# Performance work log

Measured on AMD Instinct MI355X. Metric: run time of the kernel, lower is better.

The kernel has to match this reference:

```python
import jax, jax.numpy as jnp
import numpy as np

DIM = 1024
HEADS = 16
DIM_HEAD = DIM // HEADS  # 64


def setup_inputs() -> dict:
    key = jax.random.key(0)
    k1, k2, k3 = jax.random.split(key, 3)
    x = jax.random.normal(k1, (4, 2048, DIM), dtype=jnp.float32)
    # Linear weights stored as [in, out] so y = x @ W (torch Linear uses x @ W.T; init is random either way)
    w_qkv = jax.random.normal(k2, (DIM, 3 * DIM), dtype=jnp.float32) * (DIM ** -0.5)
    w_out = jax.random.normal(k3, (DIM, DIM), dtype=jnp.float32) * (DIM ** -0.5)
    return {"x": x, "w_qkv": w_qkv, "w_out": w_out}


def reference(x, w_qkv, w_out):
    b, t, d = x.shape
    h, dh = HEADS, DIM_HEAD
    qkv = x @ w_qkv  # [b, t, 3*h*dh]
    q, k, v = jnp.split(qkv, 3, axis=-1)
    split_heads = lambda a: a.reshape(b, t, h, dh).transpose(0, 2, 1, 3)  # [b,h,t,dh]
    q, k, v = map(split_heads, (q, k, v))
    # NOTE: original scales by full model dim d, not per-head dim
    scale = d ** (-0.5)
    dots = jnp.einsum('bhie,bhje->bhij', q, k) * scale  # [b,h,t,t]
    attn = jax.nn.softmax(dots, axis=-1)
    out = jnp.einsum('bhij,bhje->bhie', attn, v)  # [b,h,t,dh]
    out = out.transpose(0, 2, 1, 3).reshape(b, t, h * dh)
    return out @ w_out
```

## Files before the change

kernel.cpp:

```cpp
#include <hip/hip_runtime.h>


typedef __bf16 bf16x8 __attribute__((ext_vector_type(8)));
typedef __bf16 bf16x4 __attribute__((ext_vector_type(4)));
typedef __bf16 bf16x2 __attribute__((ext_vector_type(2)));
typedef float f32x4 __attribute__((ext_vector_type(4)));
typedef float f32x2 __attribute__((ext_vector_type(2)));
typedef float f32x16 __attribute__((ext_vector_type(16)));
typedef unsigned short ushort8 __attribute__((ext_vector_type(8)));

#define MFMA16(a, b, c) __builtin_amdgcn_mfma_f32_16x16x32_bf16((a), (b), (c), 0, 0, 0)
#define MFMA32(a, b, c) __builtin_amdgcn_mfma_f32_32x32x16_bf16((a), (b), (c), 0, 0, 0)

__device__ __forceinline__ unsigned short f2bf(float f) {
  unsigned int u = __float_as_uint(f);
  u = (u + 0x7FFFu + ((u >> 16) & 1u)) >> 16;
  return (unsigned short)u;
}

__device__ __forceinline__ float fast_exp2(float x) {
#if __has_builtin(__builtin_amdgcn_exp2f)
  return __builtin_amdgcn_exp2f(x);
#else
  float r;
  asm("v_exp_f32 %0, %1" : "=v"(r) : "v"(x));
  return r;
#endif
}

__device__ __forceinline__ void gload_lds16(const unsigned short* g, unsigned short* l) {
  __builtin_amdgcn_global_load_lds(
      (const __attribute__((address_space(1))) unsigned int*)g,
      (__attribute__((address_space(3))) unsigned int*)l, 16, 0, 0);
}

__device__ __forceinline__ void half_swap(unsigned int a, unsigned int b,
                                          unsigned int& x, unsigned int& y,
                                          bool H) {
#if __has_builtin(__builtin_amdgcn_permlane32_swap)
  auto r = __builtin_amdgcn_permlane32_swap(a, b, false, false);
  x = (unsigned int)r[0];
  y = (unsigned int)r[1];
#else
  unsigned int oa = (unsigned int)__shfl_xor((int)a, 32);
  unsigned int ob = (unsigned int)__shfl_xor((int)b, 32);
  x = H ? ob : a;
  y = H ? b : oa;
#endif
}

__global__ __launch_bounds__(256) void prep_kernel(
    const float* __restrict__ x, unsigned short* __restrict__ xb,
    const float* __restrict__ wqkv, unsigned short* __restrict__ WqkvT,
    const float* __restrict__ wout, unsigned short* __restrict__ WoutT) {
  const int bid = blockIdx.x;
  const int tid = threadIdx.x;
  if (bid < 4096) {
    int i = (bid * 256 + tid) * 8;
    float4 a = *(const float4*)&x[i];
    float4 b = *(const float4*)&x[i + 4];
    ushort8 o = {f2bf(a.x), f2bf(a.y), f2bf(a.z), f2bf(a.w),
                 f2bf(b.x), f2bf(b.y), f2bf(b.z), f2bf(b.w)};
    *(ushort8*)&xb[i] = o;
    return;
  }
  __shared__ float t[32][33];
  const float* in;
  unsigned short* out;
  int C, scale_limit, c0, r0;
  if (bid < 4096 + 3072) {
    int tj = bid - 4096;
    in = wqkv; out = WqkvT; C = 3072; scale_limit = 1024;
    c0 = (tj % 96) * 32; r0 = (tj / 96) * 32;
  } else {
    int tj = bid - 7168;
    in = wout; out = WoutT; C = 1024; scale_limit = 0;
    c0 = (tj & 31) * 32; r0 = (tj >> 5) * 32;
  }
  const float kQScale = 0.045084220027780106f;
#pragma unroll
  for (int i = 0; i < 4; ++i) {
    int e = tid + i * 256;
    int r = e >> 5, c = e & 31;
    t[r][c] = in[(size_t)(r0 + r) * C + c0 + c];
  }
  __syncthreads();
#pragma unroll
  for (int i = 0; i < 4; ++i) {
    int e = tid + i * 256;
    int r = e >> 5, c = e & 31;
    float v = t[c][r];
    if (c0 + r < scale_limit) v *= kQScale;
    out[(size_t)(c0 + r) * 1024 + r0 + c] = f2bf(v);
  }
}

template <int MODE>
__global__ __launch_bounds__(256) void gemm_bt(
    const unsigned short* __restrict__ A, const unsigned short* __restrict__ Bt,
    void* __restrict__ Cv, unsigned short* __restrict__ VT,
    int M, int N, int K) {
  __shared__ unsigned short As[128 * 32];
  __shared__ unsigned short Bs[128 * 32];
  const int tid = threadIdx.x;
  const int wave = tid >> 6, lane = tid & 63;
  const int g = lane >> 4, ln = lane & 15;
  const int wm = wave >> 1, wn = wave & 1;
  const long bm = (long)blockIdx.y * 128;
  const long bn = (long)blockIdx.x * 128;

  f32x4 acc[4][4];
#pragma unroll
  for (int i = 0; i < 4; ++i)
#pragma unroll
    for (int j = 0; j < 4; ++j) acc[i][j] = (f32x4){0.f, 0.f, 0.f, 0.f};

  const int srow = wave * 32 + (lane >> 2);
  const int scol = (lane & 3) * 8;
  const unsigned short* gA0 = A + (bm + srow) * (long)K + scol;
  const unsigned short* gA1 = gA0 + 16 * (long)K;
  const unsigned short* gB0 = Bt + (bn + srow) * (long)K + scol;
  const unsigned short* gB1 = gB0 + 16 * (long)K;
  unsigned short* lA0 = &As[wave * 1024];
  unsigned short* lA1 = &As[wave * 1024 + 512];
  unsigned short* lB0 = &Bs[wave * 1024];
  unsigned short* lB1 = &Bs[wave * 1024 + 512];

  for (int k0 = 0; k0 < K; k0 += 32) {
    __syncthreads();
    gload_lds16(gA0 + k0, lA0);
    gload_lds16(gA1 + k0, lA1);
    gload_lds16(gB0 + k0, lB0);
    gload_lds16(gB1 + k0, lB1);
    __syncthreads();

    bf16x8 af[4], bfr[4];
#pragma unroll
    for (int i = 0; i < 4; ++i) {
      af[i]  = *(const bf16x8*)&As[(wm * 64 + i * 16 + ln) * 32 + g * 8];
      bfr[i] = *(const bf16x8*)&Bs[(wn * 64 + i * 16 + ln) * 32 + g * 8];
    }
    __builtin_amdgcn_s_setprio(1);
#pragma unroll
    for (int i = 0; i < 4; ++i)
#pragma unroll
      for (int j = 0; j < 4; ++j)
        acc[i][j] = MFMA16(af[i], bfr[j], acc[i][j]);
    __builtin_amdgcn_s_setprio(0);
  }

  const long crow = bm + wm * 64, ccol = bn + wn * 64;
  if (MODE == 2 && bn >= 2048) {
#pragma unroll
    for (int i = 0; i < 4; ++i)
#pragma unroll
      for (int j = 0; j < 4; ++j) {
        int nv = (int)(ccol + j * 16 + ln) - 2048;
        int h = nv >> 6, dh = nv & 63;
        long tg = crow + i * 16 + g * 4;
        int b = (int)(tg >> 11), tl = (int)(tg & 2047);
        size_t idx = (size_t)(b * 16 + h) * 131072 + (size_t)dh * 2048 + tl;
        bf16x4 o = {(__bf16)acc[i][j][0], (__bf16)acc[i][j][1],
                    (__bf16)acc[i][j][2], (__bf16)acc[i][j][3]};
        *(bf16x4*)&VT[idx] = o;
      }
  } else {
#pragma unroll
    for (int i = 0; i < 4; ++i)
#pragma unroll
      for (int j = 0; j < 4; ++j)
#pragma unroll
        for (int r = 0; r < 4; ++r) {
          long idx = (crow + i * 16 + g * 4 + r) * (long)N + ccol + j * 16 + ln;
          if (MODE == 1)
            ((float*)Cv)[idx] = acc[i][j][r];
          else
            ((unsigned short*)Cv)[idx] = f2bf(acc[i][j][r]);
        }
  }
}

__global__ __launch_bounds__(256, 2) void attn_kernel(
    const unsigned short* __restrict__ qkv, const unsigned short* __restrict__ VT,
    unsigned short* __restrict__ attn_out) {
  __shared__ unsigned short Ks[3][64][64];
  __shared__ unsigned short Vs[3][64][64];

  const int tid = threadIdx.x;
  const int wave = tid >> 6, lane = tid & 63;
  const int l31 = lane & 31, hb = lane >> 5;

  const int wg = (blockIdx.x & 7) * 64 + (blockIdx.x >> 3);
  const int bh = wg >> 3, qc = wg & 7;
  const int b = bh >> 4, head = bh & 15;
  const int q0 = qc * 256 + wave * 64;

  bf16x8 qfA[4], qfB[4];
  {
    size_t baseA = (size_t)(b * 2048 + q0 + l31) * 3072 + head * 64 + 8 * hb;
    size_t baseB = baseA + (size_t)32 * 3072;
    qfA[0] = *(const bf16x8*)&qkv[baseA];
    qfA[1] = *(const bf16x8*)&qkv[baseA + 16];
    qfA[2] = *(const bf16x8*)&qkv[baseA + 32];
    qfA[3] = *(const bf16x8*)&qkv[baseA + 48];
    qfB[0] = *(const bf16x8*)&qkv[baseB];
    qfB[1] = *(const bf16x8*)&qkv[baseB + 16];
    qfB[2] = *(const bf16x8*)&qkv[baseB + 32];
    qfB[3] = *(const bf16x8*)&qkv[baseB + 48];
  }

  f32x16 oaccA[2], oaccB[2];
#pragma unroll
  for (int i = 0; i < 16; ++i) {
    oaccA[0][i] = 0.f; oaccA[1][i] = 0.f;
    oaccB[0][i] = 0.f; oaccB[1][i] = 0.f;
  }
  f32x2 lsA = {0.f, 0.f}, lsB = {0.f, 0.f};

  const int srow = tid >> 3;
  const int sc = tid & 7;
  const int swz = (sc ^ (srow & 7)) * 8;
  const unsigned short* gK =
      qkv + (size_t)b * 2048 * 3072 + 1024 + head * 64 + (size_t)srow * 3072 + swz;
  const unsigned short* gV = VT + (size_t)bh * 131072 + (size_t)srow * 2048 + swz;
  const int wrow = wave * 8;

  auto STAGE = [&](int buf, int j) {
    gload_lds16(gK + (size_t)j * 3072,        &Ks[buf][wrow][0]);
    gload_lds16(gK + (size_t)(j + 32) * 3072, &Ks[buf][wrow + 32][0]);
    gload_lds16(gV + j,                       &Vs[buf][wrow][0]);
    gload_lds16(gV + 32 * 2048 + j,           &Vs[buf][wrow + 32][0]);
  };

  const int myx = l31 & 7;
  const bool H = (hb != 0);

  STAGE(0, 0);
  STAGE(1, 64);

  int idx = 0;
  for (int j0 = 0; j0 < 2048; j0 += 64) {
    if (j0 + 64 < 2048)
      asm volatile("s_waitcnt vmcnt(4)" ::: "memory");
    else
      asm volatile("s_waitcnt vmcnt(0)" ::: "memory");
    __builtin_amdgcn_s_barrier();
    __builtin_amdgcn_sched_barrier(0);
    if (j0 + 128 < 2048) {
      int nb = idx + 2; if (nb >= 3) nb -= 3;
      STAGE(nb, j0 + 128);
    }

#pragma unroll
    for (int kt = 0; kt < 2; ++kt) {
      f32x16 saA, saB;
#pragma unroll
      for (int i = 0; i < 16; ++i) { saA[i] = 0.f; saB[i] = 0.f; }
      __builtin_amdgcn_s_setprio(1);
#pragma unroll
      for (int t = 0; t < 4; ++t) {
        bf16x8 kf = *(const bf16x8*)&Ks[idx][kt * 32 + l31][((2 * t + hb) ^ myx) * 8];
        saA = MFMA32(kf, qfA[t], saA);
        saB = MFMA32(kf, qfB[t], saB);
      }
      __builtin_amdgcn_s_setprio(0);

      unsigned int pkwA[8], pkwB[8];
#pragma unroll
      for (int j = 0; j < 8; ++j) {
        float a0 = fast_exp2(saA[2 * j]);
        float a1 = fast_exp2(saA[2 * j + 1]);
        lsA += (f32x2){a0, a1};
        bf16x2 av = {(__bf16)a0, (__bf16)a1};
        pkwA[j] = __builtin_bit_cast(unsigned int, av);
        float b0 = fast_exp2(saB[2 * j]);
        float b1 = fast_exp2(saB[2 * j + 1]);
        lsB += (f32x2){b0, b1};
        bf16x2 bv = {(__bf16)b0, (__bf16)b1};
        pkwB[j] = __builtin_bit_cast(unsigned int, bv);
      }

      union { unsigned int u[4]; bf16x8 v; } pfA0, pfA1, pfB0, pfB1;
      half_swap(pkwA[0], pkwA[2], pfA0.u[0], pfA0.u[2], H);
      half_swap(pkwA[1], pkwA[3], pfA0.u[1], pfA0.u[3], H);
      half_swap(pkwA[4], pkwA[6], pfA1.u[0], pfA1.u[2], H);
      half_swap(pkwA[5], pkwA[7], pfA1.u[1], pfA1.u[3], H);
      half_swap(pkwB[0], pkwB[2], pfB0.u[0], pfB0.u[2], H);
      half_swap(pkwB[1], pkwB[3], pfB0.u[1], pfB0.u[3], H);
      half_swap(pkwB[4], pkwB[6], pfB1.u[0], pfB1.u[2], H);
      half_swap(pkwB[5], pkwB[7], pfB1.u[1], pfB1.u[3], H);

      __builtin_amdgcn_s_setprio(1);
#pragma unroll
      for (int mt = 0; mt < 2; ++mt) {
        bf16x8 vf0 = *(const bf16x8*)&Vs[idx][mt * 32 + l31][((4 * kt + hb) ^ myx) * 8];
        bf16x8 vf1 = *(const bf16x8*)&Vs[idx][mt * 32 + l31][((4 * kt + 2 + hb) ^ myx) * 8];
        oaccA[mt] = MFMA32(vf0, pfA0.v, oaccA[mt]);
        oaccA[mt] = MFMA32(vf1, pfA1.v, oaccA[mt]);
        oaccB[mt] = MFMA32(vf0, pfB0.v, oaccB[mt]);
        oaccB[mt] = MFMA32(vf1, pfB1.v, oaccB[mt]);
      }
      __builtin_amdgcn_s_setprio(0);
    }

    idx = (idx == 2) ? 0 : idx + 1;
  }

  {
    float l = lsA.x + lsA.y;
    l += __shfl_xor(l, 32);
    float inv = 1.0f / l;
    size_t row = (size_t)(b * 2048 + q0 + l31) * 1024 + head * 64;
#pragma unroll
    for (int mt = 0; mt < 2; ++mt)
#pragma unroll
      for (int rq = 0; rq < 4; ++rq) {
        bf16x4 o = {(__bf16)(oaccA[mt][4 * rq + 0] * inv),
                    (__bf16)(oaccA[mt][4 * rq + 1] * inv),
                    (__bf16)(oaccA[mt][4 * rq + 2] * inv),
                    (__bf16)(oaccA[mt][4 * rq + 3] * inv)};
        *(bf16x4*)&attn_out[row + mt * 32 + 8 * rq + 4 * hb] = o;
      }
  }
  {
    float l = lsB.x + lsB.y;
    l += __shfl_xor(l, 32);
    float inv = 1.0f / l;
    size_t row = (size_t)(b * 2048 + q0 + 32 + l31) * 1024 + head * 64;
#pragma unroll
    for (int mt = 0; mt < 2; ++mt)
#pragma unroll
      for (int rq = 0; rq < 4; ++rq) {
        bf16x4 o = {(__bf16)(oaccB[mt][4 * rq + 0] * inv),
                    (__bf16)(oaccB[mt][4 * rq + 1] * inv),
                    (__bf16)(oaccB[mt][4 * rq + 2] * inv),
                    (__bf16)(oaccB[mt][4 * rq + 3] * inv)};
        *(bf16x4*)&attn_out[row + mt * 32 + 8 * rq + 4 * hb] = o;
      }
  }
}

extern "C" void kernel_launch(void* const* d_in, const int* in_sizes, int n_in,
                              void* d_out, int out_size, void* d_ws, size_t ws_size,
                              hipStream_t stream) {
  (void)in_sizes; (void)n_in; (void)out_size; (void)ws_size;
  const float* x_f     = (const float*)d_in[0];
  const float* w_qkv_f = (const float*)d_in[1];
  const float* w_out_f = (const float*)d_in[2];
  float* out = (float*)d_out;

  char* ws = (char*)d_ws;
  unsigned short* qkv   = (unsigned short*)(ws);
  unsigned short* attn  = (unsigned short*)(ws + 50331648);
  unsigned short* VT    = (unsigned short*)(ws + 67108864);
  unsigned short* WqkvT = (unsigned short*)(ws + 83886080);
  unsigned short* WoutT = (unsigned short*)(ws + 90177536);
  unsigned short* xb    = (unsigned short*)(ws + 92274688);

  prep_kernel<<<8192, 256, 0, stream>>>(x_f, xb, w_qkv_f, WqkvT, w_out_f, WoutT);
  gemm_bt<2><<<dim3(24, 64), 256, 0, stream>>>(xb, WqkvT, qkv, VT, 8192, 3072, 1024);
  attn_kernel<<<512, 256, 0, stream>>>(qkv, VT, attn);
  gemm_bt<1><<<dim3(8, 64), 256, 0, stream>>>(attn, WoutT, out, nullptr, 8192, 1024, 1024);
}
```

Measured before the change: 183.3 us.

## Triple-buffer GEMM LDS tiles with async global-to-LDS prefetch

Replaces the single-buffered LDS tile loop in the bf16 GEMM with a three-stage ring buffer. Tiles are prefetched two k-steps ahead, with vmcnt waits and a single barrier per iteration instead of two, so global-to-LDS loads overlap the MFMA work. This triples the LDS footprint per block, which may lower occupancy, and depends on the vmcnt counting matching the four loads issued per stage.

```diff
diff --git a/kernel.cpp b/kernel.cpp
--- a/kernel.cpp
+++ b/kernel.cpp
@@ -100,8 +100,8 @@
     const unsigned short* __restrict__ A, const unsigned short* __restrict__ Bt,
     void* __restrict__ Cv, unsigned short* __restrict__ VT,
     int M, int N, int K) {
-  __shared__ unsigned short As[128 * 32];
-  __shared__ unsigned short Bs[128 * 32];
+  __shared__ unsigned short As[3 * 4096];
+  __shared__ unsigned short Bs[3 * 4096];
   const int tid = threadIdx.x;
   const int wave = tid >> 6, lane = tid & 63;
   const int g = lane >> 4, ln = lane & 15;
@@ -121,24 +121,37 @@
   const unsigned short* gA1 = gA0 + 16 * (long)K;
   const unsigned short* gB0 = Bt + (bn + srow) * (long)K + scol;
   const unsigned short* gB1 = gB0 + 16 * (long)K;
-  unsigned short* lA0 = &As[wave * 1024];
-  unsigned short* lA1 = &As[wave * 1024 + 512];
-  unsigned short* lB0 = &Bs[wave * 1024];
-  unsigned short* lB1 = &Bs[wave * 1024 + 512];
-
+
+  auto STAGE = [&](int buf, int k0) {
+    unsigned short* lA = &As[buf * 4096 + wave * 1024];
+    unsigned short* lB = &Bs[buf * 4096 + wave * 1024];
+    gload_lds16(gA0 + k0, lA);
+    gload_lds16(gA1 + k0, lA + 512);
+    gload_lds16(gB0 + k0, lB);
+    gload_lds16(gB1 + k0, lB + 512);
+  };
+
+  STAGE(0, 0);
+  STAGE(1, 32);
+
+  int bidx = 0;
   for (int k0 = 0; k0 < K; k0 += 32) {
-    __syncthreads();
-    gload_lds16(gA0 + k0, lA0);
-    gload_lds16(gA1 + k0, lA1);
-    gload_lds16(gB0 + k0, lB0);
-    gload_lds16(gB1 + k0, lB1);
-    __syncthreads();
+    if (k0 + 32 < K)
+      asm volatile("s_waitcnt vmcnt(4)" ::: "memory");
+    else
+      asm volatile("s_waitcnt vmcnt(0)" ::: "memory");
+    __builtin_amdgcn_s_barrier();
+    __builtin_amdgcn_sched_barrier(0);
+    if (k0 + 64 < K) {
+      int nb = bidx + 2; if (nb >= 3) nb -= 3;
+      STAGE(nb, k0 + 64);
+    }
 
     bf16x8 af[4], bfr[4];
 #pragma unroll
     for (int i = 0; i < 4; ++i) {
-      af[i]  = *(const bf16x8*)&As[(wm * 64 + i * 16 + ln) * 32 + g * 8];
-      bfr[i] = *(const bf16x8*)&Bs[(wn * 64 + i * 16 + ln) * 32 + g * 8];
+      af[i]  = *(const bf16x8*)&As[bidx * 4096 + (wm * 64 + i * 16 + ln) * 32 + g * 8];
+      bfr[i] = *(const bf16x8*)&Bs[bidx * 4096 + (wn * 64 + i * 16 + ln) * 32 + g * 8];
     }
     __builtin_amdgcn_s_setprio(1);
 #pragma unroll
@@ -147,6 +160,8 @@
       for (int j = 0; j < 4; ++j)
         acc[i][j] = MFMA16(af[i], bfr[j], acc[i][j]);
     __builtin_amdgcn_s_setprio(0);
+
+    bidx = (bidx == 2) ? 0 : bidx + 1;
   }
 
   const long crow = bm + wm * 64, ccol = bn + wn * 64;
```

Result: faster. 178.9 us (median of 2 runs) (-2.4%).
